# Kernel optimization log

Measured on AMD Instinct MI355X. Metric: run time of the kernel, lower is better.

The kernel has to match this reference:

```python
import jax, jax.numpy as jnp
import numpy as np

K = 3          # kernel_size
BOARD = 15     # gomoku board H = W
HOUT = BOARD - K + 1   # 13 windows per spatial dim
DIM_IN = 2 * K * K     # 18 binary features per window -> perfect hash


def fake_quant(x, scale, bits=8):
    """Straight-through fake quantization: round to int grid, clamp to bit range."""
    qmax = 2 ** (bits - 1) - 1
    y = jnp.clip(jnp.round(x * scale), -qmax - 1, qmax) / scale
    return x + jax.lax.stop_gradient(y - x)


def setup_inputs() -> dict:
    key = jax.random.key(0)
    ks = jax.random.split(key, 8)
    B = 8192
    board = jax.random.randint(ks[0], (B, 2, BOARD, BOARD), 0, 2, dtype=jnp.int32)
    emb = jax.random.normal(ks[1], (2 ** 18, 32), dtype=jnp.float32) * 0.05
    w1 = jax.random.normal(ks[2], (32, 32), dtype=jnp.float32) * 0.1
    b1 = jax.random.normal(ks[3], (32,), dtype=jnp.float32) * 0.05
    w2 = jax.random.normal(ks[4], (32, 32), dtype=jnp.float32) * 0.1
    b2 = jax.random.normal(ks[5], (32,), dtype=jnp.float32) * 0.05
    w3 = jax.random.normal(ks[6], (3, 32), dtype=jnp.float32) * 0.1
    b3 = jax.random.normal(ks[7], (3,), dtype=jnp.float32) * 0.05
    return {"board": board, "emb": emb, "w1": w1, "b1": b1,
            "w2": w2, "b2": b2, "w3": w3, "b3": b3}


def reference(board, emb, w1, b1, w2, b2, w3, b3):
    B = board.shape[0]
    # im2col unfold in torch F.unfold order (channel-major, then kernel row, col)
    # patches: (B, HOUT, HOUT, C*K*K)
    patches = jnp.stack(
        [board[:, c, i:i + HOUT, j:j + HOUT]
         for c in range(2) for i in range(K) for j in range(K)], axis=-1)
    # perfect hash of 18 binary features -> index into 2^18 embedding table
    powers = (2 ** jnp.arange(DIM_IN)).astype(jnp.int32)
    idx = jnp.sum(patches * powers, axis=-1)          # (B, HOUT, HOUT)
    feats = emb[idx]                                  # (B, HOUT, HOUT, 32) gather
    feats = fake_quant(jnp.clip(feats, -1.0, 127 / 128), 128.0, bits=8)
    v = jnp.sum(feats, axis=(1, 2))                   # (B, 32) clamp-sum accumulate
    # tiny quantized 3-layer value MLP
    for i, (wt, bs) in enumerate(((w1, b1), (w2, b2), (w3, b3))):
        v = jnp.clip(v, -1.0 if i == 0 else 0.0, 127 / 128)
        wq = fake_quant(wt, 128.0, bits=8)
        bq = fake_quant(bs, 128.0 * 128.0, bits=32)
        v = v @ wq.T + bq
    policy = jnp.zeros((B, BOARD, BOARD), dtype=v.dtype)
    return (v, policy)
```

## Files before the change

kernel.cpp:

```cpp
#include <hip/hip_runtime.h>
#include <stdint.h>

#define NW 169

__device__ __forceinline__ float qw128(float x) {
    float r = rintf(x * 128.f);
    r = fminf(fmaxf(r, -128.f), 127.f);
    return r * 0.0078125f;
}
__device__ __forceinline__ float qb16384(float x) {
    return rintf(x * 16384.f) * 6.103515625e-05f;
}

__global__ void nnue_kernel(const int* __restrict__ board,
                            const float* __restrict__ emb,
                            const float* __restrict__ w1, const float* __restrict__ b1,
                            const float* __restrict__ w2, const float* __restrict__ b2,
                            const float* __restrict__ w3, const float* __restrict__ b3,
                            float* __restrict__ vout, float4* __restrict__ policy)
{
    int tid = threadIdx.x;
    if (blockIdx.x >= 2048) {
        int i = (blockIdx.x - 2048) * 256 + tid;
        policy[i] = make_float4(0.f, 0.f, 0.f, 0.f);
        return;
    }

    __shared__ float w1T[32][32], w2T[32][32], w3T[32][4];
    __shared__ float b1q[32], b2q[32], b3q[4];
    __shared__ unsigned long long ballots[4][8];
    __shared__ int hashidx[4][176];
    __shared__ float vlds[4][32], h1lds[4][32], h2lds[4][32];

    for (int i = tid; i < 1024; i += 256) {
        int j = i & 31, k = i >> 5;
        w1T[k][j] = qw128(w1[j * 32 + k]);
        w2T[k][j] = qw128(w2[j * 32 + k]);
    }
    if (tid < 96) { int k = tid & 31, j = tid >> 5; w3T[k][j] = qw128(w3[j * 32 + k]); }
    if (tid < 32) { b1q[tid] = qb16384(b1[tid]); b2q[tid] = qb16384(b2[tid]); }
    if (tid < 3)  b3q[tid] = qb16384(b3[tid]);
    __syncthreads();

    int wv = tid >> 6, lane = tid & 63;
    int b = blockIdx.x * 4 + wv;
    const int* bp = board + b * 450;

#pragma unroll
    for (int t = 0; t < 8; ++t) {
        int n = t * 64 + lane;
        int cell = (n < 450) ? bp[n] : 0;
        unsigned long long m = __ballot(cell != 0);
        if (lane == 0) ballots[wv][t] = m;
    }

#pragma unroll
    for (int t = 0; t < 3; ++t) {
        int w = t * 64 + lane;
        if (w < NW) {
            int wi = w / 13;
            int wj = w - wi * 13;
            int idx = 0;
#pragma unroll
            for (int c = 0; c < 2; ++c) {
#pragma unroll
                for (int i = 0; i < 3; ++i) {
                    int s = c * 225 + (wi + i) * 15;
                    int word = s >> 6, off = s & 63;
                    unsigned long long lo = ballots[wv][word];
                    unsigned long long hi = ballots[wv][word + 1];
                    unsigned long long bits = (lo >> off) | ((hi << 1) << (63 - off));
                    idx |= (int)((bits >> wj) & 7ull) << (9 * c + 3 * i);
                }
            }
            hashidx[wv][w] = idx;
        }
    }

    int c0 = lane & 7;
    int g = lane >> 3;
    const float* basef = emb + c0 * 4;
    float a0 = 0.f, a1 = 0.f, a2 = 0.f, a3 = 0.f;
#pragma unroll 4
    for (int it = 0; it < 22; ++it) {
        int w = it * 8 + g;
        if (w < NW) {
            int idx = hashidx[wv][w];
            float4 f = *(const float4*)(basef + (size_t)idx * 32);
            a0 += rintf(fminf(fmaxf(f.x, -1.f), 0.9921875f) * 128.f);
            a1 += rintf(fminf(fmaxf(f.y, -1.f), 0.9921875f) * 128.f);
            a2 += rintf(fminf(fmaxf(f.z, -1.f), 0.9921875f) * 128.f);
            a3 += rintf(fminf(fmaxf(f.w, -1.f), 0.9921875f) * 128.f);
        }
    }
#pragma unroll
    for (int off = 8; off <= 32; off <<= 1) {
        a0 += __shfl_xor(a0, off);
        a1 += __shfl_xor(a1, off);
        a2 += __shfl_xor(a2, off);
        a3 += __shfl_xor(a3, off);
    }
    if (lane < 8) {
        vlds[wv][lane * 4 + 0] = fminf(fmaxf(a0, -128.f), 127.f) * 0.0078125f;
        vlds[wv][lane * 4 + 1] = fminf(fmaxf(a1, -128.f), 127.f) * 0.0078125f;
        vlds[wv][lane * 4 + 2] = fminf(fmaxf(a2, -128.f), 127.f) * 0.0078125f;
        vlds[wv][lane * 4 + 3] = fminf(fmaxf(a3, -128.f), 127.f) * 0.0078125f;
    }

    int jj = lane & 31, hf = lane >> 5;
    float s1 = 0.f;
#pragma unroll
    for (int k2 = 0; k2 < 16; ++k2) {
        int k = hf * 16 + k2;
        s1 = fmaf(vlds[wv][k], w1T[k][jj], s1);
    }
    s1 += __shfl_xor(s1, 32);
    s1 += b1q[jj];
    s1 = fminf(fmaxf(s1, 0.f), 0.9921875f);
    if (lane < 32) h1lds[wv][jj] = s1;

    float s2 = 0.f;
#pragma unroll
    for (int k2 = 0; k2 < 16; ++k2) {
        int k = hf * 16 + k2;
        s2 = fmaf(h1lds[wv][k], w2T[k][jj], s2);
    }
    s2 += __shfl_xor(s2, 32);
    s2 += b2q[jj];
    s2 = fminf(fmaxf(s2, 0.f), 0.9921875f);
    if (lane < 32) h2lds[wv][jj] = s2;

    float s3 = 0.f;
    if (jj < 3) {
#pragma unroll
        for (int k2 = 0; k2 < 16; ++k2) {
            int k = hf * 16 + k2;
            s3 = fmaf(h2lds[wv][k], w3T[k][jj], s3);
        }
    }
    s3 += __shfl_xor(s3, 32);
    if (lane < 3) vout[b * 3 + lane] = s3 + b3q[lane];
}

extern "C" void kernel_launch(void* const* d_in, const int* in_sizes, int n_in,
                              void* d_out, int out_size, void* d_ws, size_t ws_size,
                              hipStream_t stream) {
    const int*   board = (const int*)d_in[0];
    const float* emb   = (const float*)d_in[1];
    const float* w1    = (const float*)d_in[2];
    const float* b1    = (const float*)d_in[3];
    const float* w2    = (const float*)d_in[4];
    const float* b2    = (const float*)d_in[5];
    const float* w3    = (const float*)d_in[6];
    const float* b3    = (const float*)d_in[7];
    float* out = (float*)d_out;

    nnue_kernel<<<3848, 256, 0, stream>>>(board, emb, w1, b1, w2, b2, w3, b3,
                                          out, (float4*)(out + 24576));
}
```

Measured before the change: 41.05 us.

## Prequantize embedding table to uint8 planes and split into prep/gather/MLP kernels

A prep kernel quantizes the whole 2^18x32 float embedding table into two offset uint8 planes of 16 bytes per row, and packs board ballots into a workspace. The gather kernel then fetches 16-byte rows per window and sums them with packed-integer SIMD-within-register adds and wave shuffles; a separate MLP kernel finishes the network. This shrinks the random-gather footprint fourfold, but every call now reads the full 32 MB table and writes 8 MB, and pays for three launches.

```diff
diff --git a/kernel.cpp b/kernel.cpp
--- a/kernel.cpp
+++ b/kernel.cpp
@@ -2,6 +2,8 @@
 #include <stdint.h>
 
 #define NW 169
+
+typedef float f32x4 __attribute__((ext_vector_type(4)));
 
 __device__ __forceinline__ float qw128(float x) {
     float r = rintf(x * 128.f);
@@ -12,26 +14,136 @@
     return rintf(x * 16384.f) * 6.103515625e-05f;
 }
 
-__global__ void nnue_kernel(const int* __restrict__ board,
-                            const float* __restrict__ emb,
-                            const float* __restrict__ w1, const float* __restrict__ b1,
-                            const float* __restrict__ w2, const float* __restrict__ b2,
-                            const float* __restrict__ w3, const float* __restrict__ b3,
-                            float* __restrict__ vout, float4* __restrict__ policy)
+__global__ __launch_bounds__(256)
+void prep_kernel(const float* __restrict__ emb, uint8_t* __restrict__ plane0,
+                 uint8_t* __restrict__ plane1,
+                 const int* __restrict__ board, unsigned long long* __restrict__ bb)
 {
-    int tid = threadIdx.x;
-    if (blockIdx.x >= 2048) {
-        int i = (blockIdx.x - 2048) * 256 + tid;
-        policy[i] = make_float4(0.f, 0.f, 0.f, 0.f);
+    int bid = blockIdx.x, tid = threadIdx.x;
+    if (bid < 1024) {
+        int row = bid * 256 + tid;
+        const float4* in4 = (const float4*)emb + (size_t)row * 8;
+        uint32_t w[8];
+#pragma unroll
+        for (int t = 0; t < 8; ++t) {
+            float4 f = in4[t];
+            float v[4] = {f.x, f.y, f.z, f.w};
+            uint32_t u = 0;
+#pragma unroll
+            for (int j = 0; j < 4; ++j) {
+                float x = fminf(fmaxf(v[j], -1.f), 0.9921875f);
+                int r = (int)rintf(x * 128.f) + 128;
+                u |= ((uint32_t)r & 0xFFu) << (8 * j);
+            }
+            w[t] = u;
+        }
+        ((uint4*)plane0)[row] = make_uint4(w[0], w[1], w[2], w[3]);
+        ((uint4*)plane1)[row] = make_uint4(w[4], w[5], w[6], w[7]);
         return;
     }
-
+    int wv = tid >> 6, lane = tid & 63;
+    int b = (bid - 1024) * 4 + wv;
+    const int* bp = board + (size_t)b * 450;
+#pragma unroll
+    for (int t = 0; t < 8; ++t) {
+        int n = t * 64 + lane;
+        int cell = (n < 450) ? bp[n] : 0;
+        unsigned long long m = __ballot(cell != 0);
+        if (lane == 0) bb[(size_t)b * 8 + t] = m;
+    }
+}
+
+__global__ __launch_bounds__(256)
+void gather_kernel(const unsigned long long* __restrict__ bb,
+                   const uint8_t* __restrict__ plane0,
+                   const uint8_t* __restrict__ plane1,
+                   float* __restrict__ vhalf, f32x4* __restrict__ policy)
+{
+    int bid = blockIdx.x, tid = threadIdx.x;
+    if (bid < 1800) {
+        int i = bid * 256 + tid;
+        f32x4 z = {0.f, 0.f, 0.f, 0.f};
+        __builtin_nontemporal_store(z, &policy[i]);
+        return;
+    }
+    __shared__ unsigned long long ballots[4][8];
+    int gb = bid - 1800;
+    int p = gb & 1;
+    int wv = tid >> 6, lane = tid & 63;
+    int b = (gb >> 1) * 4 + wv;
+    if (lane < 8) ballots[wv][lane] = bb[(size_t)b * 8 + lane];
+    const uint8_t* plane = p ? plane1 : plane0;
+
+    int off[3];
+#pragma unroll
+    for (int r = 0; r < 3; ++r) {
+        int w = r * 64 + lane;
+        int wc = min(w, NW - 1);
+        int wi = wc / 13, wj = wc - wi * 13;
+        int idx = 0;
+#pragma unroll
+        for (int c = 0; c < 2; ++c) {
+#pragma unroll
+            for (int i = 0; i < 3; ++i) {
+                int s = c * 225 + (wi + i) * 15;
+                int word = s >> 6, o = s & 63;
+                unsigned long long lo = ballots[wv][word];
+                unsigned long long hi = ballots[wv][word + 1];
+                unsigned long long bits = (lo >> o) | ((hi << 1) << (63 - o));
+                idx |= (int)((bits >> wj) & 7ull) << (9 * c + 3 * i);
+            }
+        }
+        off[r] = idx * 16;
+    }
+
+    uint4 d0 = *(const uint4*)(plane + off[0]);
+    uint4 d1 = *(const uint4*)(plane + off[1]);
+    uint4 d2 = *(const uint4*)(plane + off[2]);
+    uint32_t k2m = (128 + lane < NW) ? 0xFFFFFFFFu : 0u;
+    d2.x &= k2m; d2.y &= k2m; d2.z &= k2m; d2.w &= k2m;
+
+    const uint32_t M = 0x00FF00FFu;
+    uint32_t lo0 = (d0.x & M) + (d1.x & M) + (d2.x & M);
+    uint32_t hi0 = ((d0.x >> 8) & M) + ((d1.x >> 8) & M) + ((d2.x >> 8) & M);
+    uint32_t lo1 = (d0.y & M) + (d1.y & M) + (d2.y & M);
+    uint32_t hi1 = ((d0.y >> 8) & M) + ((d1.y >> 8) & M) + ((d2.y >> 8) & M);
+    uint32_t lo2 = (d0.z & M) + (d1.z & M) + (d2.z & M);
+    uint32_t hi2 = ((d0.z >> 8) & M) + ((d1.z >> 8) & M) + ((d2.z >> 8) & M);
+    uint32_t lo3 = (d0.w & M) + (d1.w & M) + (d2.w & M);
+    uint32_t hi3 = ((d0.w >> 8) & M) + ((d1.w >> 8) & M) + ((d2.w >> 8) & M);
+
+#pragma unroll
+    for (int o = 1; o <= 32; o <<= 1) {
+        lo0 += __shfl_xor(lo0, o); hi0 += __shfl_xor(hi0, o);
+        lo1 += __shfl_xor(lo1, o); hi1 += __shfl_xor(hi1, o);
+        lo2 += __shfl_xor(lo2, o); hi2 += __shfl_xor(hi2, o);
+        lo3 += __shfl_xor(lo3, o); hi3 += __shfl_xor(hi3, o);
+    }
+
+    if (lane < 16) {
+        int j = lane >> 2, pos = lane & 3;
+        uint32_t wl = (j == 0) ? lo0 : (j == 1) ? lo1 : (j == 2) ? lo2 : lo3;
+        uint32_t wh = (j == 0) ? hi0 : (j == 1) ? hi1 : (j == 2) ? hi2 : hi3;
+        uint32_t src = (pos & 1) ? wh : wl;
+        uint32_t val = (pos >= 2) ? (src >> 16) : (src & 0xFFFFu);
+        int s = (int)val - 21632;
+        s = min(max(s, -128), 127);
+        vhalf[(size_t)b * 32 + p * 16 + lane] = (float)s * 0.0078125f;
+    }
+}
+
+__global__ __launch_bounds__(256)
+void mlp_kernel(const float* __restrict__ vhalf,
+                const float* __restrict__ w1, const float* __restrict__ b1,
+                const float* __restrict__ w2, const float* __restrict__ b2,
+                const float* __restrict__ w3, const float* __restrict__ b3,
+                float* __restrict__ vout)
+{
     __shared__ float w1T[32][32], w2T[32][32], w3T[32][4];
     __shared__ float b1q[32], b2q[32], b3q[4];
-    __shared__ unsigned long long ballots[4][8];
-    __shared__ int hashidx[4][176];
-    __shared__ float vlds[4][32], h1lds[4][32], h2lds[4][32];
-
+    __shared__ float vlds[8][32], h1lds[8][32], h2lds[8][32];
+
+    int tid = threadIdx.x;
     for (int i = tid; i < 1024; i += 256) {
         int j = i & 31, k = i >> 5;
         w1T[k][j] = qw128(w1[j * 32 + k]);
@@ -43,103 +155,39 @@
     __syncthreads();
 
     int wv = tid >> 6, lane = tid & 63;
-    int b = blockIdx.x * 4 + wv;
-    const int* bp = board + b * 450;
-
-#pragma unroll
-    for (int t = 0; t < 8; ++t) {
-        int n = t * 64 + lane;
-        int cell = (n < 450) ? bp[n] : 0;
-        unsigned long long m = __ballot(cell != 0);
-        if (lane == 0) ballots[wv][t] = m;
-    }
-
-#pragma unroll
-    for (int t = 0; t < 3; ++t) {
-        int w = t * 64 + lane;
-        if (w < NW) {
-            int wi = w / 13;
-            int wj = w - wi * 13;
-            int idx = 0;
-#pragma unroll
-            for (int c = 0; c < 2; ++c) {
-#pragma unroll
-                for (int i = 0; i < 3; ++i) {
-                    int s = c * 225 + (wi + i) * 15;
-                    int word = s >> 6, off = s & 63;
-                    unsigned long long lo = ballots[wv][word];
-                    unsigned long long hi = ballots[wv][word + 1];
-                    unsigned long long bits = (lo >> off) | ((hi << 1) << (63 - off));
-                    idx |= (int)((bits >> wj) & 7ull) << (9 * c + 3 * i);
-                }
-            }
-            hashidx[wv][w] = idx;
+    int bbase = blockIdx.x * 8;
+    int jj = lane & 31, hf = lane >> 5;
+
+#pragma unroll
+    for (int rb = 0; rb < 2; ++rb) {
+        int s = wv * 2 + rb;
+        int b = bbase + s;
+        if (lane < 32) vlds[s][lane] = vhalf[(size_t)b * 32 + lane];
+
+        float t1 = 0.f;
+#pragma unroll
+        for (int k2 = 0; k2 < 16; ++k2) { int k = hf * 16 + k2; t1 = fmaf(vlds[s][k], w1T[k][jj], t1); }
+        t1 += __shfl_xor(t1, 32);
+        t1 += b1q[jj];
+        t1 = fminf(fmaxf(t1, 0.f), 0.9921875f);
+        if (lane < 32) h1lds[s][jj] = t1;
+
+        float t2 = 0.f;
+#pragma unroll
+        for (int k2 = 0; k2 < 16; ++k2) { int k = hf * 16 + k2; t2 = fmaf(h1lds[s][k], w2T[k][jj], t2); }
+        t2 += __shfl_xor(t2, 32);
+        t2 += b2q[jj];
+        t2 = fminf(fmaxf(t2, 0.f), 0.9921875f);
+        if (lane < 32) h2lds[s][jj] = t2;
+
+        float t3 = 0.f;
+        if (jj < 3) {
+#pragma unroll
+            for (int k2 = 0; k2 < 16; ++k2) { int k = hf * 16 + k2; t3 = fmaf(h2lds[s][k], w3T[k][jj], t3); }
         }
-    }
-
-    int c0 = lane & 7;
-    int g = lane >> 3;
-    const float* basef = emb + c0 * 4;
-    float a0 = 0.f, a1 = 0.f, a2 = 0.f, a3 = 0.f;
-#pragma unroll 4
-    for (int it = 0; it < 22; ++it) {
-        int w = it * 8 + g;
-        if (w < NW) {
-            int idx = hashidx[wv][w];
-            float4 f = *(const float4*)(basef + (size_t)idx * 32);
-            a0 += rintf(fminf(fmaxf(f.x, -1.f), 0.9921875f) * 128.f);
-            a1 += rintf(fminf(fmaxf(f.y, -1.f), 0.9921875f) * 128.f);
-            a2 += rintf(fminf(fmaxf(f.z, -1.f), 0.9921875f) * 128.f);
-            a3 += rintf(fminf(fmaxf(f.w, -1.f), 0.9921875f) * 128.f);
-        }
-    }
-#pragma unroll
-    for (int off = 8; off <= 32; off <<= 1) {
-        a0 += __shfl_xor(a0, off);
-        a1 += __shfl_xor(a1, off);
-        a2 += __shfl_xor(a2, off);
-        a3 += __shfl_xor(a3, off);
-    }
-    if (lane < 8) {
-        vlds[wv][lane * 4 + 0] = fminf(fmaxf(a0, -128.f), 127.f) * 0.0078125f;
-        vlds[wv][lane * 4 + 1] = fminf(fmaxf(a1, -128.f), 127.f) * 0.0078125f;
-        vlds[wv][lane * 4 + 2] = fminf(fmaxf(a2, -128.f), 127.f) * 0.0078125f;
-        vlds[wv][lane * 4 + 3] = fminf(fmaxf(a3, -128.f), 127.f) * 0.0078125f;
-    }
-
-    int jj = lane & 31, hf = lane >> 5;
-    float s1 = 0.f;
-#pragma unroll
-    for (int k2 = 0; k2 < 16; ++k2) {
-        int k = hf * 16 + k2;
-        s1 = fmaf(vlds[wv][k], w1T[k][jj], s1);
-    }
-    s1 += __shfl_xor(s1, 32);
-    s1 += b1q[jj];
-    s1 = fminf(fmaxf(s1, 0.f), 0.9921875f);
-    if (lane < 32) h1lds[wv][jj] = s1;
-
-    float s2 = 0.f;
-#pragma unroll
-    for (int k2 = 0; k2 < 16; ++k2) {
-        int k = hf * 16 + k2;
-        s2 = fmaf(h1lds[wv][k], w2T[k][jj], s2);
-    }
-    s2 += __shfl_xor(s2, 32);
-    s2 += b2q[jj];
-    s2 = fminf(fmaxf(s2, 0.f), 0.9921875f);
-    if (lane < 32) h2lds[wv][jj] = s2;
-
-    float s3 = 0.f;
-    if (jj < 3) {
-#pragma unroll
-        for (int k2 = 0; k2 < 16; ++k2) {
-            int k = hf * 16 + k2;
-            s3 = fmaf(h2lds[wv][k], w3T[k][jj], s3);
-        }
-    }
-    s3 += __shfl_xor(s3, 32);
-    if (lane < 3) vout[b * 3 + lane] = s3 + b3q[lane];
+        t3 += __shfl_xor(t3, 32);
+        if (lane < 3) vout[(size_t)b * 3 + lane] = t3 + b3q[lane];
+    }
 }
 
 extern "C" void kernel_launch(void* const* d_in, const int* in_sizes, int n_in,
@@ -155,6 +203,13 @@
     const float* b3    = (const float*)d_in[7];
     float* out = (float*)d_out;
 
-    nnue_kernel<<<3848, 256, 0, stream>>>(board, emb, w1, b1, w2, b2, w3, b3,
-                                          out, (float4*)(out + 24576));
-}
+    uint8_t* plane0 = (uint8_t*)d_ws;
+    uint8_t* plane1 = plane0 + (1u << 22);
+    unsigned long long* bb = (unsigned long long*)(plane0 + (1u << 23));
+    float* vhalf = (float*)(plane0 + (9u << 20));
+
+    prep_kernel  <<<3072, 256, 0, stream>>>(emb, plane0, plane1, board, bb);
+    gather_kernel<<<5896, 256, 0, stream>>>(bb, plane0, plane1, vhalf,
+                                            (f32x4*)(out + 24576));
+    mlp_kernel   <<<1024, 256, 0, stream>>>(vhalf, w1, b1, w2, b2, w3, b3, out);
+}
```

After: 43.94 us. 7.0% more time.
